# Kernel tuning notes

Measured on AMD Instinct MI355X. Metric: run time of the kernel, lower is better.

## Reference

```python
import jax, jax.numpy as jnp
import numpy as np

B, N, D = 4, 4096, 512
K = 16384          # codebook size
NUM_Q = 2          # residual quantizers (shared codebook)


def setup_inputs() -> dict:
    key = jax.random.key(0)
    ks = jax.random.split(key, 6)
    s = 1.0 / np.sqrt(D)
    return {
        "x": jax.random.normal(ks[0], (B, N, D), dtype=jnp.float32),
        "enc_w": jax.random.normal(ks[1], (D, D), dtype=jnp.float32) * s,
        "enc_b": jnp.zeros((D,), dtype=jnp.float32),
        "codebook": jax.random.normal(ks[2], (K, D), dtype=jnp.float32),
        "dec_w": jax.random.normal(ks[3], (D, D), dtype=jnp.float32) * s,
        "dec_b": jnp.zeros((D,), dtype=jnp.float32),
    }


def _residual_vq(z, codebook):
    # z: [B, N, D] -> flatten tokens
    flat = z.reshape(-1, z.shape[-1])          # [T, D]
    c_sq = jnp.sum(codebook * codebook, axis=-1)  # [K]
    q_sum = jnp.zeros_like(flat)
    residual = flat
    for _ in range(NUM_Q):
        # argmin of ||r - c||^2 == argmin of (||c||^2 - 2 r.c); skip ||r||^2
        dists = c_sq[None, :] - 2.0 * (residual @ codebook.T)  # [T, K]
        idx = jnp.argmin(dists, axis=-1)                       # [T]
        q = codebook[idx]                                      # gather [T, D]
        q_sum = q_sum + q
        residual = residual - q
    return q_sum.reshape(z.shape)


def reference(x, enc_w, enc_b, codebook, dec_w, dec_b):
    z = x @ enc_w.T + enc_b                     # encoder Linear(512 -> 512)
    q = _residual_vq(z, codebook)               # sum of per-stage code vectors
    z_tilde = z + jax.lax.stop_gradient(q - z)  # straight-through estimator
    x_recon = z_tilde @ dec_w.T + dec_b         # decoder Linear(512 -> 512)
    return x_recon
```

## Files before the change

kernel.cpp:

```cpp
#include <hip/hip_runtime.h>
#include <stdint.h>

constexpr int TT = 16384;
constexpr int DD = 512;
constexpr int KK = 16384;
constexpr int TOPK = 8;

typedef __bf16 bf16x8 __attribute__((ext_vector_type(8)));
typedef __bf16 bf16x4 __attribute__((ext_vector_type(4)));
typedef float f32x4 __attribute__((ext_vector_type(4)));

typedef const __attribute__((address_space(1))) void* gas_ptr;
typedef __attribute__((address_space(3))) void* las_ptr;

__device__ __forceinline__ unsigned long long pack_di(float d, int idx) {
    uint32_t u = __float_as_uint(d);
    u = (u & 0x80000000u) ? ~u : (u | 0x80000000u);
    return ((unsigned long long)u << 32) | (uint32_t)idx;
}

__device__ __forceinline__ unsigned long long umin64(unsigned long long a,
                                                     unsigned long long b) {
    return a < b ? a : b;
}

template<int MODE>
__global__ __launch_bounds__(256)
void gemm_mfma(const float* __restrict__ A, const float* __restrict__ A2,
               const float* __restrict__ W, const float* __restrict__ bias,
               float* __restrict__ out0, float* __restrict__ out1,
               __bf16* __restrict__ out2)
{
    __shared__ __bf16 Ah[128 * 64], Al[128 * 64];
    __shared__ __bf16 Bh[128 * 64], Bl[128 * 64];
    const int tid = threadIdx.x;
    const int lane = tid & 63;
    const int w = tid >> 6;
    const int row0 = blockIdx.y * 128;
    const int col0 = blockIdx.x * 128;

    f32x4 acc[2][8] = {};

    const int sr = tid >> 4;
    const int scol = (tid & 15) * 4;
    const int lcol = (((scol >> 3) ^ (sr & 7)) << 3) + (scol & 7);

    int a_off[2], b_off[8];
    #pragma unroll
    for (int mi = 0; mi < 2; ++mi) {
        const int ar = w * 32 + mi * 16 + (lane & 15);
        a_off[mi] = ar * 64 + (((lane >> 4) ^ (ar & 7)) << 3);
    }
    #pragma unroll
    for (int ni = 0; ni < 8; ++ni) {
        const int br = ni * 16 + (lane & 15);
        b_off[ni] = br * 64 + (((lane >> 4) ^ (br & 7)) << 3);
    }

    for (int kb = 0; kb < 512; kb += 64) {
        __syncthreads();
        #pragma unroll
        for (int i = 0; i < 8; ++i) {
            const int r = i * 16 + sr;
            float4 v = *(const float4*)(A + (size_t)(row0 + r) * 512 + kb + scol);
            if (MODE == 1) {
                const float4 u = *(const float4*)(A2 + (size_t)(row0 + r) * 512 + kb + scol);
                v.x -= u.x; v.y -= u.y; v.z -= u.z; v.w -= u.w;
            }
            bf16x4 hv, lv;
            hv[0] = (__bf16)v.x; hv[1] = (__bf16)v.y; hv[2] = (__bf16)v.z; hv[3] = (__bf16)v.w;
            lv[0] = (__bf16)(v.x - (float)hv[0]); lv[1] = (__bf16)(v.y - (float)hv[1]);
            lv[2] = (__bf16)(v.z - (float)hv[2]); lv[3] = (__bf16)(v.w - (float)hv[3]);
            *(bf16x4*)(Ah + r * 64 + lcol) = hv;
            *(bf16x4*)(Al + r * 64 + lcol) = lv;

            const float4 x = *(const float4*)(W + (size_t)(col0 + r) * 512 + kb + scol);
            bf16x4 hw, lw;
            hw[0] = (__bf16)x.x; hw[1] = (__bf16)x.y; hw[2] = (__bf16)x.z; hw[3] = (__bf16)x.w;
            lw[0] = (__bf16)(x.x - (float)hw[0]); lw[1] = (__bf16)(x.y - (float)hw[1]);
            lw[2] = (__bf16)(x.z - (float)hw[2]); lw[3] = (__bf16)(x.w - (float)hw[3]);
            *(bf16x4*)(Bh + r * 64 + lcol) = hw;
            *(bf16x4*)(Bl + r * 64 + lcol) = lw;
        }
        __syncthreads();
        #pragma unroll
        for (int s = 0; s < 2; ++s) {
            const int sx = s * 32;
            bf16x8 ah[2], al[2];
            #pragma unroll
            for (int mi = 0; mi < 2; ++mi) {
                ah[mi] = *(const bf16x8*)(Ah + (a_off[mi] ^ sx));
                al[mi] = *(const bf16x8*)(Al + (a_off[mi] ^ sx));
            }
            #pragma unroll
            for (int ni = 0; ni < 8; ++ni) {
                const bf16x8 bh = *(const bf16x8*)(Bh + (b_off[ni] ^ sx));
                const bf16x8 bl = *(const bf16x8*)(Bl + (b_off[ni] ^ sx));
                #pragma unroll
                for (int mi = 0; mi < 2; ++mi) {
                    acc[mi][ni] = __builtin_amdgcn_mfma_f32_16x16x32_bf16(ah[mi], bh, acc[mi][ni], 0, 0, 0);
                    acc[mi][ni] = __builtin_amdgcn_mfma_f32_16x16x32_bf16(ah[mi], bl, acc[mi][ni], 0, 0, 0);
                    acc[mi][ni] = __builtin_amdgcn_mfma_f32_16x16x32_bf16(al[mi], bh, acc[mi][ni], 0, 0, 0);
                }
            }
        }
    }

    #pragma unroll
    for (int mi = 0; mi < 2; ++mi) {
        #pragma unroll
        for (int reg = 0; reg < 4; ++reg) {
            const int row = row0 + w * 32 + mi * 16 + (lane >> 4) * 4 + reg;
            #pragma unroll
            for (int ni = 0; ni < 8; ++ni) {
                const int col = col0 + ni * 16 + (lane & 15);
                const float o = acc[mi][ni][reg] + bias[col];
                out0[(size_t)row * 512 + col] = o;
                if (MODE == 0) {
                    out1[(size_t)row * 512 + col] = o;
                    out2[(size_t)row * 512 + col] = (__bf16)o;
                }
            }
        }
    }
}

__global__ __launch_bounds__(256)
void dist_approx(const __bf16* __restrict__ Rh,
                 const __bf16* __restrict__ Ch,
                 const float* __restrict__ csq,
                 unsigned long long* __restrict__ winners)
{
    __shared__ __bf16 As[128 * 64];
    __shared__ __bf16 Bs[256 * 64];
    const int tid = threadIdx.x;
    const int lane = tid & 63;
    const int w = tid >> 6;
    const int wm = w >> 1, wn = w & 1;
    const int row0 = blockIdx.y * 128;
    const int col0 = blockIdx.x * 256;

    f32x4 acc[4][8] = {};

    const int gc = (lane & 7) ^ ((lane >> 3) & 7);
    const __bf16* Ab = Rh + (size_t)(row0 + w * 32 + (lane >> 3)) * 512 + gc * 8;
    const __bf16* Bb = Ch + (size_t)(col0 + w * 64 + (lane >> 3)) * 512 + gc * 8;
    __bf16* lA = As + (w * 32) * 64;
    __bf16* lB = Bs + (w * 64) * 64;

    int a_off[4], b_off[8];
    #pragma unroll
    for (int mi = 0; mi < 4; ++mi) {
        const int ar = wm * 64 + mi * 16 + (lane & 15);
        a_off[mi] = ar * 64 + (((lane >> 4) ^ (ar & 7)) << 3);
    }
    #pragma unroll
    for (int ni = 0; ni < 8; ++ni) {
        const int br = wn * 128 + ni * 16 + (lane & 15);
        b_off[ni] = br * 64 + (((lane >> 4) ^ (br & 7)) << 3);
    }

    for (int kb = 0; kb < 512; kb += 64) {
        __syncthreads();
        #pragma unroll
        for (int j = 0; j < 4; ++j)
            __builtin_amdgcn_global_load_lds(
                (gas_ptr)(Ab + (size_t)j * 8 * 512 + kb), (las_ptr)(lA + j * 8 * 64), 16, 0, 0);
        #pragma unroll
        for (int j = 0; j < 8; ++j)
            __builtin_amdgcn_global_load_lds(
                (gas_ptr)(Bb + (size_t)j * 8 * 512 + kb), (las_ptr)(lB + j * 8 * 64), 16, 0, 0);
        __syncthreads();
        #pragma unroll
        for (int s = 0; s < 2; ++s) {
            const int sx = s * 32;
            bf16x8 af[4], bfr[8];
            #pragma unroll
            for (int mi = 0; mi < 4; ++mi) af[mi] = *(const bf16x8*)(As + (a_off[mi] ^ sx));
            #pragma unroll
            for (int ni = 0; ni < 8; ++ni) bfr[ni] = *(const bf16x8*)(Bs + (b_off[ni] ^ sx));
            #pragma unroll
            for (int mi = 0; mi < 4; ++mi)
                #pragma unroll
                for (int ni = 0; ni < 8; ++ni)
                    acc[mi][ni] = __builtin_amdgcn_mfma_f32_16x16x32_bf16(
                        af[mi], bfr[ni], acc[mi][ni], 0, 0, 0);
        }
    }

    float csv[8];
    #pragma unroll
    for (int ni = 0; ni < 8; ++ni)
        csv[ni] = csq[col0 + wn * 128 + ni * 16 + (lane & 15)];

    const int tile = blockIdx.x * 2 + wn;
    #pragma unroll
    for (int mi = 0; mi < 4; ++mi) {
        #pragma unroll
        for (int reg = 0; reg < 4; ++reg) {
            unsigned long long b = ~0ull, s = ~0ull;
            #pragma unroll
            for (int ni = 0; ni < 8; ++ni) {
                const float d = fmaf(-2.0f, acc[mi][ni][reg], csv[ni]);
                const unsigned long long x =
                    pack_di(d, col0 + wn * 128 + ni * 16 + (lane & 15));
                const unsigned long long nb = umin64(b, x);
                s = umin64(s, b ^ x ^ nb);
                b = nb;
            }
            #pragma unroll
            for (int m = 1; m < 16; m <<= 1) {
                const unsigned long long ob = __shfl_xor(b, m, 16);
                const unsigned long long os = __shfl_xor(s, m, 16);
                const unsigned long long nb = umin64(b, ob);
                s = umin64(umin64(s, os), b ^ ob ^ nb);
                b = nb;
            }
            if ((lane & 15) == 0) {
                const int row = row0 + wm * 64 + mi * 16 + (lane >> 4) * 4 + reg;
                winners[(size_t)row * 256 + tile * 2 + 0] = b;
                winners[(size_t)row * 256 + tile * 2 + 1] = s;
            }
        }
    }
}

__global__ __launch_bounds__(256)
void select_rescore(const unsigned long long* __restrict__ winners,
                    const float* __restrict__ CB, const float* __restrict__ csq,
                    float* __restrict__ R, __bf16* __restrict__ R16)
{
    const int w = threadIdx.x >> 6;
    const int lane = threadIdx.x & 63;
    const int token = blockIdx.x * 4 + w;

    const unsigned long long* wt = winners + (size_t)token * 256;
    unsigned long long v[4];
    #pragma unroll
    for (int j = 0; j < 4; ++j) v[j] = wt[lane * 4 + j];

    unsigned long long cand[TOPK];
    #pragma unroll
    for (int t = 0; t < TOPK; ++t) {
        unsigned long long mm = umin64(umin64(v[0], v[1]), umin64(v[2], v[3]));
        #pragma unroll
        for (int m = 1; m < 64; m <<= 1)
            mm = umin64(mm, __shfl_xor(mm, m, 64));
        cand[t] = mm;
        #pragma unroll
        for (int j = 0; j < 4; ++j) if (v[j] == mm) v[j] = ~0ull;
    }

    float4 r0 = *(const float4*)(R + (size_t)token * 512 + lane * 8);
    float4 r1 = *(const float4*)(R + (size_t)token * 512 + lane * 8 + 4);

    unsigned long long best = ~0ull;
    #pragma unroll
    for (int t = 0; t < TOPK; ++t) {
        const int col = (int)(cand[t] & 0xFFFFFFFFull);
        const float4 c0 = *(const float4*)(CB + (size_t)col * 512 + lane * 8);
        const float4 c1 = *(const float4*)(CB + (size_t)col * 512 + lane * 8 + 4);
        float dot = r0.x * c0.x;
        dot = fmaf(r0.y, c0.y, dot); dot = fmaf(r0.z, c0.z, dot);
        dot = fmaf(r0.w, c0.w, dot); dot = fmaf(r1.x, c1.x, dot);
        dot = fmaf(r1.y, c1.y, dot); dot = fmaf(r1.z, c1.z, dot);
        dot = fmaf(r1.w, c1.w, dot);
        #pragma unroll
        for (int m = 1; m < 64; m <<= 1) dot += __shfl_xor(dot, m, 64);
        const float d = fmaf(-2.0f, dot, csq[col]);
        best = umin64(best, pack_di(d, col));
    }

    const int bcol = (int)(best & 0xFFFFFFFFull);
    const float4 c0 = *(const float4*)(CB + (size_t)bcol * 512 + lane * 8);
    const float4 c1 = *(const float4*)(CB + (size_t)bcol * 512 + lane * 8 + 4);
    r0.x -= c0.x; r0.y -= c0.y; r0.z -= c0.z; r0.w -= c0.w;
    r1.x -= c1.x; r1.y -= c1.y; r1.z -= c1.z; r1.w -= c1.w;
    *(float4*)(R + (size_t)token * 512 + lane * 8) = r0;
    *(float4*)(R + (size_t)token * 512 + lane * 8 + 4) = r1;
    bf16x8 h;
    h[0] = (__bf16)r0.x; h[1] = (__bf16)r0.y; h[2] = (__bf16)r0.z; h[3] = (__bf16)r0.w;
    h[4] = (__bf16)r1.x; h[5] = (__bf16)r1.y; h[6] = (__bf16)r1.z; h[7] = (__bf16)r1.w;
    *(bf16x8*)(R16 + (size_t)token * 512 + lane * 8) = h;
}

__global__ __launch_bounds__(256)
void prep_cb(const float* __restrict__ CB, float* __restrict__ c_sq,
             __bf16* __restrict__ cb16)
{
    const int wave = threadIdx.x >> 6;
    const int lane = threadIdx.x & 63;
    const int row = blockIdx.x * 4 + wave;
    const float* p = CB + (size_t)row * DD + lane * 8;
    const float4 a = *(const float4*)p;
    const float4 b = *(const float4*)(p + 4);
    bf16x8 h;
    h[0] = (__bf16)a.x; h[1] = (__bf16)a.y; h[2] = (__bf16)a.z; h[3] = (__bf16)a.w;
    h[4] = (__bf16)b.x; h[5] = (__bf16)b.y; h[6] = (__bf16)b.z; h[7] = (__bf16)b.w;
    *(bf16x8*)(cb16 + (size_t)row * DD + lane * 8) = h;
    float s = a.x*a.x + a.y*a.y + a.z*a.z + a.w*a.w
            + b.x*b.x + b.y*b.y + b.z*b.z + b.w*b.w;
    #pragma unroll
    for (int m = 1; m < 64; m <<= 1) s += __shfl_xor(s, m, 64);
    if (lane == 0) c_sq[row] = s;
}

extern "C" void kernel_launch(void* const* d_in, const int* in_sizes, int n_in,
                              void* d_out, int out_size, void* d_ws, size_t ws_size,
                              hipStream_t stream)
{
    const float* x    = (const float*)d_in[0];
    const float* encw = (const float*)d_in[1];
    const float* encb = (const float*)d_in[2];
    const float* cb   = (const float*)d_in[3];
    const float* decw = (const float*)d_in[4];
    const float* decb = (const float*)d_in[5];
    float* out = (float*)d_out;

    float* z    = (float*)d_ws;
    float* r    = z + (size_t)TT * DD;
    __bf16* cb16 = (__bf16*)(r + (size_t)TT * DD);
    __bf16* r16  = cb16 + (size_t)KK * DD;
    float* csq  = (float*)(r16 + (size_t)TT * DD);
    unsigned long long* winners = (unsigned long long*)d_out;

    const dim3 blk(256);

    gemm_mfma<0><<<dim3(DD / 128, TT / 128), blk, 0, stream>>>(
        x, nullptr, encw, encb, z, r, r16);

    prep_cb<<<dim3(KK / 4), blk, 0, stream>>>(cb, csq, cb16);

    for (int s = 0; s < 2; ++s) {
        dist_approx<<<dim3(KK / 256, TT / 128), blk, 0, stream>>>(r16, cb16, csq, winners);
        select_rescore<<<dim3(TT / 4), blk, 0, stream>>>(winners, cb, csq, r, r16);
    }

    gemm_mfma<1><<<dim3(DD / 128, TT / 128), blk, 0, stream>>>(
        z, r, decw, decb, out, nullptr, nullptr);
}
```

Before: 1.142 ms.

## Shrink distance tile to 128x128 and pack top-2 keys into 32 bits

The distance GEMM tile shrinks from 128x256 with K-step 64 to 128x128 with K-step 32, which cuts accumulator registers and LDS per block and should raise occupancy. The cost is less operand reuse and twice as many barrier-separated K iterations. Per-tile top-2 candidates become 32-bit keys: a sortable distance with its low 6 bits replaced by the local column. This halves the shuffle width and store size, but the twice-as-many winner entries per token are rebuilt into 64-bit keys in the select kernel. Dropping the low mantissa bits coarsens the ordering, though exact fp32 rescoring of the top-8 should tolerate it.

```diff
diff --git a/kernel.cpp b/kernel.cpp
--- a/kernel.cpp
+++ b/kernel.cpp
@@ -22,6 +22,13 @@
 __device__ __forceinline__ unsigned long long umin64(unsigned long long a,
                                                      unsigned long long b) {
     return a < b ? a : b;
+}
+__device__ __forceinline__ uint32_t umin32(uint32_t a, uint32_t b) { return a < b ? a : b; }
+__device__ __forceinline__ uint32_t umax32(uint32_t a, uint32_t b) { return a > b ? a : b; }
+
+__device__ __forceinline__ uint32_t sortable(float d) {
+    uint32_t u = __float_as_uint(d);
+    return u ^ ((uint32_t)((int32_t)u >> 31) | 0x80000000u);
 }
 
 template<int MODE>
@@ -129,104 +136,101 @@
 void dist_approx(const __bf16* __restrict__ Rh,
                  const __bf16* __restrict__ Ch,
                  const float* __restrict__ csq,
-                 unsigned long long* __restrict__ winners)
-{
-    __shared__ __bf16 As[128 * 64];
-    __shared__ __bf16 Bs[256 * 64];
+                 uint32_t* __restrict__ winners)
+{
+    __shared__ __bf16 As[128 * 32];
+    __shared__ __bf16 Bs[128 * 32];
     const int tid = threadIdx.x;
     const int lane = tid & 63;
     const int w = tid >> 6;
     const int wm = w >> 1, wn = w & 1;
     const int row0 = blockIdx.y * 128;
-    const int col0 = blockIdx.x * 256;
-
-    f32x4 acc[4][8] = {};
-
-    const int gc = (lane & 7) ^ ((lane >> 3) & 7);
-    const __bf16* Ab = Rh + (size_t)(row0 + w * 32 + (lane >> 3)) * 512 + gc * 8;
-    const __bf16* Bb = Ch + (size_t)(col0 + w * 64 + (lane >> 3)) * 512 + gc * 8;
-    __bf16* lA = As + (w * 32) * 64;
-    __bf16* lB = Bs + (w * 64) * 64;
-
-    int a_off[4], b_off[8];
+    const int col0 = blockIdx.x * 128;
+
+    f32x4 acc[4][4] = {};
+
+    const int srow0 = w * 32 + (lane >> 2);
+    const int srow1 = srow0 + 16;
+    const int gc0 = (lane & 3) ^ ((srow0 >> 1) & 3);
+    const int gc1 = (lane & 3) ^ ((srow1 >> 1) & 3);
+    __bf16* ldsA0 = As + (w * 32 + 0) * 32;
+    __bf16* ldsA1 = As + (w * 32 + 16) * 32;
+    __bf16* ldsB0 = Bs + (w * 32 + 0) * 32;
+    __bf16* ldsB1 = Bs + (w * 32 + 16) * 32;
+
+    int a_off[4], b_off[4];
+    #pragma unroll
+    for (int i = 0; i < 4; ++i) {
+        const int ar = wm * 64 + i * 16 + (lane & 15);
+        a_off[i] = ar * 32 + (((lane >> 4) ^ ((ar >> 1) & 3)) << 3);
+        const int br = wn * 64 + i * 16 + (lane & 15);
+        b_off[i] = br * 32 + (((lane >> 4) ^ ((br >> 1) & 3)) << 3);
+    }
+
+    for (int kb = 0; kb < 512; kb += 32) {
+        __syncthreads();
+        __builtin_amdgcn_global_load_lds(
+            (gas_ptr)(Rh + (size_t)(row0 + srow0) * 512 + kb + gc0 * 8), (las_ptr)ldsA0, 16, 0, 0);
+        __builtin_amdgcn_global_load_lds(
+            (gas_ptr)(Rh + (size_t)(row0 + srow1) * 512 + kb + gc1 * 8), (las_ptr)ldsA1, 16, 0, 0);
+        __builtin_amdgcn_global_load_lds(
+            (gas_ptr)(Ch + (size_t)(col0 + srow0) * 512 + kb + gc0 * 8), (las_ptr)ldsB0, 16, 0, 0);
+        __builtin_amdgcn_global_load_lds(
+            (gas_ptr)(Ch + (size_t)(col0 + srow1) * 512 + kb + gc1 * 8), (las_ptr)ldsB1, 16, 0, 0);
+        __syncthreads();
+
+        bf16x8 af[4], bfr[4];
+        #pragma unroll
+        for (int i = 0; i < 4; ++i) af[i]  = *(const bf16x8*)(As + a_off[i]);
+        #pragma unroll
+        for (int i = 0; i < 4; ++i) bfr[i] = *(const bf16x8*)(Bs + b_off[i]);
+        #pragma unroll
+        for (int mi = 0; mi < 4; ++mi)
+            #pragma unroll
+            for (int ni = 0; ni < 4; ++ni)
+                acc[mi][ni] = __builtin_amdgcn_mfma_f32_16x16x32_bf16(
+                    af[mi], bfr[ni], acc[mi][ni], 0, 0, 0);
+    }
+
+    float csv[4];
+    #pragma unroll
+    for (int ni = 0; ni < 4; ++ni)
+        csv[ni] = csq[col0 + wn * 64 + ni * 16 + (lane & 15)];
+
+    const int tile = blockIdx.x * 2 + wn;
     #pragma unroll
     for (int mi = 0; mi < 4; ++mi) {
-        const int ar = wm * 64 + mi * 16 + (lane & 15);
-        a_off[mi] = ar * 64 + (((lane >> 4) ^ (ar & 7)) << 3);
-    }
-    #pragma unroll
-    for (int ni = 0; ni < 8; ++ni) {
-        const int br = wn * 128 + ni * 16 + (lane & 15);
-        b_off[ni] = br * 64 + (((lane >> 4) ^ (br & 7)) << 3);
-    }
-
-    for (int kb = 0; kb < 512; kb += 64) {
-        __syncthreads();
-        #pragma unroll
-        for (int j = 0; j < 4; ++j)
-            __builtin_amdgcn_global_load_lds(
-                (gas_ptr)(Ab + (size_t)j * 8 * 512 + kb), (las_ptr)(lA + j * 8 * 64), 16, 0, 0);
-        #pragma unroll
-        for (int j = 0; j < 8; ++j)
-            __builtin_amdgcn_global_load_lds(
-                (gas_ptr)(Bb + (size_t)j * 8 * 512 + kb), (las_ptr)(lB + j * 8 * 64), 16, 0, 0);
-        __syncthreads();
-        #pragma unroll
-        for (int s = 0; s < 2; ++s) {
-            const int sx = s * 32;
-            bf16x8 af[4], bfr[8];
-            #pragma unroll
-            for (int mi = 0; mi < 4; ++mi) af[mi] = *(const bf16x8*)(As + (a_off[mi] ^ sx));
-            #pragma unroll
-            for (int ni = 0; ni < 8; ++ni) bfr[ni] = *(const bf16x8*)(Bs + (b_off[ni] ^ sx));
-            #pragma unroll
-            for (int mi = 0; mi < 4; ++mi)
-                #pragma unroll
-                for (int ni = 0; ni < 8; ++ni)
-                    acc[mi][ni] = __builtin_amdgcn_mfma_f32_16x16x32_bf16(
-                        af[mi], bfr[ni], acc[mi][ni], 0, 0, 0);
-        }
-    }
-
-    float csv[8];
-    #pragma unroll
-    for (int ni = 0; ni < 8; ++ni)
-        csv[ni] = csq[col0 + wn * 128 + ni * 16 + (lane & 15)];
-
-    const int tile = blockIdx.x * 2 + wn;
-    #pragma unroll
-    for (int mi = 0; mi < 4; ++mi) {
         #pragma unroll
         for (int reg = 0; reg < 4; ++reg) {
-            unsigned long long b = ~0ull, s = ~0ull;
-            #pragma unroll
-            for (int ni = 0; ni < 8; ++ni) {
+            uint32_t b = 0xFFFFFFFFu, s = 0xFFFFFFFFu;
+            #pragma unroll
+            for (int ni = 0; ni < 4; ++ni) {
                 const float d = fmaf(-2.0f, acc[mi][ni][reg], csv[ni]);
-                const unsigned long long x =
-                    pack_di(d, col0 + wn * 128 + ni * 16 + (lane & 15));
-                const unsigned long long nb = umin64(b, x);
-                s = umin64(s, b ^ x ^ nb);
+                const uint32_t key = (sortable(d) & 0xFFFFFFC0u)
+                                   | (uint32_t)(ni * 16 + (lane & 15));
+                const uint32_t nb = umin32(b, key);
+                s = umin32(s, umax32(b, key));
                 b = nb;
             }
             #pragma unroll
             for (int m = 1; m < 16; m <<= 1) {
-                const unsigned long long ob = __shfl_xor(b, m, 16);
-                const unsigned long long os = __shfl_xor(s, m, 16);
-                const unsigned long long nb = umin64(b, ob);
-                s = umin64(umin64(s, os), b ^ ob ^ nb);
+                const uint32_t ob = __shfl_xor((int)b, m, 16);
+                const uint32_t os = __shfl_xor((int)s, m, 16);
+                const uint32_t nb = umin32(b, ob);
+                s = umin32(umin32(s, os), umax32(b, ob));
                 b = nb;
             }
             if ((lane & 15) == 0) {
                 const int row = row0 + wm * 64 + mi * 16 + (lane >> 4) * 4 + reg;
-                winners[(size_t)row * 256 + tile * 2 + 0] = b;
-                winners[(size_t)row * 256 + tile * 2 + 1] = s;
+                uint2 v; v.x = b; v.y = s;
+                *(uint2*)(winners + (size_t)row * 512 + tile * 2) = v;
             }
         }
     }
 }
 
 __global__ __launch_bounds__(256)
-void select_rescore(const unsigned long long* __restrict__ winners,
+void select_rescore(const uint32_t* __restrict__ winners,
                     const float* __restrict__ CB, const float* __restrict__ csq,
                     float* __restrict__ R, __bf16* __restrict__ R16)
 {
@@ -234,21 +238,30 @@
     const int lane = threadIdx.x & 63;
     const int token = blockIdx.x * 4 + w;
 
-    const unsigned long long* wt = winners + (size_t)token * 256;
-    unsigned long long v[4];
-    #pragma unroll
-    for (int j = 0; j < 4; ++j) v[j] = wt[lane * 4 + j];
+    const uint32_t* wt = winners + (size_t)token * 512;
+    uint4 q0 = *(const uint4*)(wt + lane * 8);
+    uint4 q1 = *(const uint4*)(wt + lane * 8 + 4);
+    uint32_t k32[8] = {q0.x, q0.y, q0.z, q0.w, q1.x, q1.y, q1.z, q1.w};
+
+    unsigned long long v[8];
+    #pragma unroll
+    for (int j = 0; j < 8; ++j) {
+        const int gcol = ((lane * 8 + j) >> 1) * 64 + (int)(k32[j] & 63u);
+        v[j] = ((unsigned long long)k32[j] << 32) | (uint32_t)gcol;
+    }
 
     unsigned long long cand[TOPK];
     #pragma unroll
     for (int t = 0; t < TOPK; ++t) {
-        unsigned long long mm = umin64(umin64(v[0], v[1]), umin64(v[2], v[3]));
+        unsigned long long mm = v[0];
+        #pragma unroll
+        for (int j = 1; j < 8; ++j) mm = umin64(mm, v[j]);
         #pragma unroll
         for (int m = 1; m < 64; m <<= 1)
             mm = umin64(mm, __shfl_xor(mm, m, 64));
         cand[t] = mm;
         #pragma unroll
-        for (int j = 0; j < 4; ++j) if (v[j] == mm) v[j] = ~0ull;
+        for (int j = 0; j < 8; ++j) if (v[j] == mm) v[j] = ~0ull;
     }
 
     float4 r0 = *(const float4*)(R + (size_t)token * 512 + lane * 8);
@@ -322,7 +335,7 @@
     __bf16* cb16 = (__bf16*)(r + (size_t)TT * DD);
     __bf16* r16  = cb16 + (size_t)KK * DD;
     float* csq  = (float*)(r16 + (size_t)TT * DD);
-    unsigned long long* winners = (unsigned long long*)d_out;
+    uint32_t* winners = (uint32_t*)d_out;
 
     const dim3 blk(256);
 
@@ -332,7 +345,7 @@
     prep_cb<<<dim3(KK / 4), blk, 0, stream>>>(cb, csq, cb16);
 
     for (int s = 0; s < 2; ++s) {
-        dist_approx<<<dim3(KK / 256, TT / 128), blk, 0, stream>>>(r16, cb16, csq, winners);
+        dist_approx<<<dim3(KK / 128, TT / 128), blk, 0, stream>>>(r16, cb16, csq, winners);
         select_rescore<<<dim3(TT / 4), blk, 0, stream>>>(winners, cb, csq, r, r16);
     }
 
```

Result: faster. 1.090 ms (-4.5%).
